# Optimization experiments

Hardware: AMD Instinct MI355X
Metric: run time of the kernel (lower is better)

The kernel has to match this reference:

```python
import jax, jax.numpy as jnp
import numpy as np

LAM = 0.1   # smooth_param
EPS = 1e-8  # torch cosine_similarity eps


def setup_inputs() -> dict:
    key = jax.random.key(0)
    k1, k2, k3 = jax.random.split(key, 3)
    B, num_supp, num_query, T, D = 8, 5, 128, 16, 2048
    supp = jax.random.normal(k1, (B, num_supp, T, D), jnp.float32)
    query = jax.random.normal(k2, (B, num_query, T, D), jnp.float32)
    query_ys = jax.random.randint(k3, (B * num_query,), 0, num_supp)
    return {"supp": supp, "query": query, "query_ys": query_ys}


def _cosine_dist(supp, query):
    # supp: (B, ns, T, D), query: (B, nq, T, D)
    # dist[b,q,s,l,m] = 1 - cos(supp[b,s,l], query[b,q,m]); batch order (b,q,s)
    B, ns, T, D = supp.shape
    nq = query.shape[1]
    dots = jnp.einsum('bsld,bqmd->bqslm', supp, query)
    sn = jnp.linalg.norm(supp, axis=-1)   # (B, ns, T)
    qn = jnp.linalg.norm(query, axis=-1)  # (B, nq, T)
    denom = jnp.maximum(sn[:, None, :, :, None] * qn[:, :, None, None, :], EPS)
    dist = 1.0 - dots / denom
    return dist.reshape(B * nq * ns, T, T)


def _dtw(dist):
    # Relaxed (soft-min) OTAM band DP. dist: (N, T, T) -> (N,)
    # opt grid is (T, T+2) with zero-padded columns m=0 and m=T+1.
    N, T, _ = dist.shape
    dist_pad = jnp.pad(dist, ((0, 0), (0, 0), (1, 1)))  # (N, T, T+2)
    # Row l=0: opt[0,m] = cumsum of dist_pad[0, :m+1]
    row0 = jnp.cumsum(dist_pad[:, 0, :], axis=-1)  # (N, T+2)

    m_idx = jnp.arange(1, T + 2)
    boundary = (m_idx == 1) | (m_idx == T + 1)  # 3-way softmin only at band edges

    def row_step(prev_row, dist_row):
        # prev_row: (N, T+2) = opt[l-1]; dist_row: (N, T+2) = dist_pad[:, l]
        def col_step(left, xs):
            diag, up, d, is_b = xs  # each (N,) except is_b scalar bool
            s2 = jnp.logaddexp(-diag / LAM, -left / LAM)        # {diag, left}
            s3 = jnp.logaddexp(s2, -up / LAM)                   # + {up}
            val = -LAM * jnp.where(is_b, s3, s2) + d
            return val, val

        xs = (prev_row[:, :-1].T, prev_row[:, 1:].T, dist_row[:, 1:].T, boundary)
        init = jnp.zeros((N,), dist_row.dtype)  # opt[l, 0] = 0
        _, cols = jax.lax.scan(col_step, init, xs)  # (T+1, N)
        new_row = jnp.concatenate([init[:, None], cols.T], axis=1)  # (N, T+2)
        return new_row, None

    rows = jnp.swapaxes(dist_pad[:, 1:, :], 0, 1)  # (T-1, N, T+2)
    final_row, _ = jax.lax.scan(row_step, row0, rows)
    return final_row[:, -1]  # opt[:, T-1, T+1]


def _cross_entropy(logits, labels):
    logp = jax.nn.log_softmax(logits, axis=-1)
    return -jnp.mean(jnp.take_along_axis(logp, labels[:, None], axis=1))


def reference(supp, query, query_ys):
    ns = supp.shape[1]
    dist = _cosine_dist(supp, query)            # (B*nq*ns, T, T)
    tam1 = _dtw(dist).reshape(-1, ns)           # forward-direction alignment
    tam2 = _dtw(dist[:, ::-1, ::-1]).reshape(-1, ns)  # flipped (dims 1,2)
    loss1 = _cross_entropy(-tam1, query_ys)
    loss2 = _cross_entropy(-tam2, query_ys)
    loss = 0.5 * (loss1 + loss2)
    tam = 0.5 * (tam1 + tam2)
    return loss, tam
```

## Files before the change

### kernel.cpp

```cpp
#include <hip/hip_runtime.h>
#include <hip/hip_bf16.h>

#define NB   8
#define NS   5
#define NQ   128
#define TT   16
#define DD   2048
#define NROW 1024
#define NSROW (NB * NS * TT)
#define LDB  2056
#define LAMI 10.0f
#define LAMF 0.1f

typedef __attribute__((ext_vector_type(8))) short  short8;
typedef __attribute__((ext_vector_type(4))) float  float4v;

static __device__ __forceinline__ unsigned int f2bf2(float x, float y) {
    union { float f; unsigned int u; } a, b; a.f = x; b.f = y;
    unsigned int ra = a.u + 0x7fffu + ((a.u >> 16) & 1u);
    unsigned int rb = b.u + 0x7fffu + ((b.u >> 16) & 1u);
    return (ra >> 16) | (rb & 0xffff0000u);
}

static __device__ __forceinline__ float lse2f(float x, float y) {
    float mx = fmaxf(x, y), mn = fminf(x, y);
    return mx + __logf(1.0f + __expf(mn - mx));
}

__global__ __launch_bounds__(256) void
preproc_supp(const float* __restrict__ supp, unsigned short* __restrict__ suppBf,
             float* __restrict__ suppSq)
{
    const int wave = threadIdx.x >> 6, lane = threadIdx.x & 63;
    const int row = blockIdx.x * 4 + wave;
    const float* src = supp + (size_t)row * DD;
    unsigned short* dst = suppBf + (size_t)row * DD;
    float ss = 0.f;
    #pragma unroll
    for (int i = 0; i < 8; ++i) {
        float4 v = *reinterpret_cast<const float4*>(src + i * 256 + lane * 4);
        uint2 pv = { f2bf2(v.x, v.y), f2bf2(v.z, v.w) };
        *reinterpret_cast<uint2*>(dst + i * 256 + lane * 4) = pv;
        ss += v.x * v.x + v.y * v.y + v.z * v.z + v.w * v.w;
    }
    #pragma unroll
    for (int off = 32; off >= 1; off >>= 1) ss += __shfl_xor(ss, off, 64);
    if (lane == 0) suppSq[row] = ss;
}

__global__ __launch_bounds__(512, 4) void
dist_dtw_kernel(const unsigned short* __restrict__ suppBf, const float* __restrict__ suppSq,
                const float* __restrict__ query,
                float* __restrict__ out_tam, float* __restrict__ t1w, float* __restrict__ t2w)
{
    __shared__ __align__(16) unsigned short sB[TT * LDB];
    __shared__ float ssq[96];
    __shared__ float distS[NS][TT][TT];
    __shared__ float tamv[16];

    const int tid  = threadIdx.x;
    const int blk  = blockIdx.x;
    const int wave = tid >> 6;
    const int lane = tid & 63;
    const int fr   = lane & 15;
    const int quad = lane >> 4;

    {
        const int r = tid >> 5;
        const int c = tid & 31;
        const float* src = query + (size_t)(blk * TT + r) * DD;
        float ss = 0.f;
        #pragma unroll
        for (int i = 0; i < 16; ++i) {
            float4 v = *reinterpret_cast<const float4*>(src + (c + i * 32) * 4);
            uint2 pv = { f2bf2(v.x, v.y), f2bf2(v.z, v.w) };
            *reinterpret_cast<uint2*>(&sB[r * LDB + (c + i * 32) * 4]) = pv;
            ss += v.x * v.x + v.y * v.y + v.z * v.z + v.w * v.w;
        }
        #pragma unroll
        for (int off = 16; off >= 1; off >>= 1) ss += __shfl_xor(ss, off, 32);
        if ((tid & 31) == 0) ssq[80 + r] = ss;
        if (tid < 80) ssq[tid] = suppSq[(blk >> 7) * (NS * TT) + tid];
    }
    __syncthreads();

    float4v acc0 = {0.f, 0.f, 0.f, 0.f}, acc1 = {0.f, 0.f, 0.f, 0.f};
    if (wave < NS) {
        const unsigned short* ap =
            suppBf + ((size_t)((blk >> 7) * NS + wave) * TT + fr) * DD + quad * 8;
        const unsigned short* bp = &sB[fr * LDB + quad * 8];
        #pragma unroll 8
        for (int k = 0; k < 64; k += 2) {
            short8 a0 = *reinterpret_cast<const short8*>(ap + k * 32);
            short8 a1 = *reinterpret_cast<const short8*>(ap + k * 32 + 32);
            short8 b0 = *reinterpret_cast<const short8*>(bp + k * 32);
            short8 b1 = *reinterpret_cast<const short8*>(bp + k * 32 + 32);
            acc0 = __builtin_amdgcn_mfma_f32_16x16x32_bf16(a0, b0, acc0, 0, 0, 0);
            acc1 = __builtin_amdgcn_mfma_f32_16x16x32_bf16(a1, b1, acc1, 0, 0, 0);
        }
        float qn = sqrtf(ssq[80 + fr]);
        #pragma unroll
        for (int r = 0; r < 4; ++r) {
            int l = quad * 4 + r;
            float denom = fmaxf(sqrtf(ssq[wave * 16 + l]) * qn, 1e-8f);
            distS[wave][l][fr] = 1.0f - (acc0[r] + acc1[r]) / denom;
        }
    }
    __syncthreads();

    if (wave < NS && (lane & 31) <= 17) {
        const int g   = lane & 31;
        const int dir = lane >> 5;
        const int s   = wave;
        float val = 0.f, vprev = 0.f;
        #pragma unroll
        for (int t = 1; t <= 32; ++t) {
            float left = __shfl_up(val,   1, 32);
            float diag = __shfl_up(vprev, 1, 32);
            int l = t - g;
            if (g >= 1 && l >= 0 && l <= 15) {
                float d = 0.f;
                if (g <= 16) d = dir ? distS[s][15 - l][16 - g] : distS[s][l][g - 1];
                float nv;
                if (l == 0) {
                    nv = left + d;
                } else if (g == 1 || g == 17) {
                    nv = -LAMF * lse2f(lse2f(-diag * LAMI, -left * LAMI), -val * LAMI) + d;
                } else {
                    float lo2 = fminf(diag, left), hi2 = fmaxf(diag, left);
                    nv = lo2 - LAMF * __logf(1.0f + __expf((lo2 - hi2) * LAMI)) + d;
                }
                vprev = val; val = nv;
            }
        }
        if (g == 17) tamv[s * 2 + dir] = val;
    }
    __syncthreads();

    if (tid < NS) {
        float t1 = tamv[2 * tid], t2 = tamv[2 * tid + 1];
        int n = blk * NS + tid;
        t1w[n] = t1;
        t2w[n] = t2;
        out_tam[n] = 0.5f * (t1 + t2);
    }
}

__global__ __launch_bounds__(1024) void
loss_kernel(const float* __restrict__ t1w, const float* __restrict__ t2w,
            const int* __restrict__ ys, float* __restrict__ out)
{
    __shared__ float red[16];
    const int row = threadIdx.x;

    float t1[NS], t2[NS];
    #pragma unroll
    for (int s = 0; s < NS; ++s) { t1[s] = t1w[row * NS + s]; t2[s] = t2w[row * NS + s]; }
    const int y = ys[row];

    float mx1 = -t1[0], mx2 = -t2[0];
    #pragma unroll
    for (int s = 1; s < NS; ++s) { mx1 = fmaxf(mx1, -t1[s]); mx2 = fmaxf(mx2, -t2[s]); }
    float s1 = 0.f, s2 = 0.f;
    #pragma unroll
    for (int s = 0; s < NS; ++s) { s1 += __expf(-t1[s] - mx1); s2 += __expf(-t2[s] - mx2); }
    float lse1  = mx1 + __logf(s1);
    float lse2v = mx2 + __logf(s2);

    float ty1 = t1[0], ty2 = t2[0];
    #pragma unroll
    for (int s = 1; s < NS; ++s) { if (y == s) { ty1 = t1[s]; ty2 = t2[s]; } }

    float c = 0.5f * ((lse1 + ty1) + (lse2v + ty2));

    #pragma unroll
    for (int off = 32; off >= 1; off >>= 1) c += __shfl_down(c, off, 64);
    if ((row & 63) == 0) red[row >> 6] = c;
    __syncthreads();
    if (row == 0) {
        float tot = 0.f;
        #pragma unroll
        for (int i = 0; i < 16; ++i) tot += red[i];
        out[0] = tot * (1.0f / (float)NROW);
    }
}

extern "C" void kernel_launch(void* const* d_in, const int* in_sizes, int n_in,
                              void* d_out, int out_size, void* d_ws, size_t ws_size,
                              hipStream_t stream) {
    const float* supp  = (const float*)d_in[0];
    const float* query = (const float*)d_in[1];
    const int*   ys    = (const int*)d_in[2];
    float* out = (float*)d_out;

    float* t1w    = (float*)d_ws;
    float* t2w    = t1w + NROW * NS;
    float* suppSq = t2w + NROW * NS;
    unsigned short* suppBf = (unsigned short*)(suppSq + NSROW);

    preproc_supp<<<NSROW / 4, 256, 0, stream>>>(supp, suppBf, suppSq);
    dist_dtw_kernel<<<NROW, 512, 0, stream>>>(suppBf, suppSq, query, out + 1, t1w, t2w);
    loss_kernel<<<1, 1024, 0, stream>>>(t1w, t2w, ys, out);
}
```

Measured before the change: 254.6 us.

## Halve query LDS staging to raise occupancy and fuse loss via atomics

The query tile is now staged in LDS in two halves of the D dimension rather than all at once. This halves the shared-memory footprint so the launch bound can allow 8 blocks per CU instead of 4, at the cost of extra barriers between the two halves. The separate loss kernel is removed. Each DTW block computes its row's cross-entropy term and atomically adds it to the output, which preproc_supp zeroes first. This saves a launch and a workspace round trip, but the floating-point atomics make the summation order nondeterministic.

```diff
diff --git a/kernel.cpp b/kernel.cpp
--- a/kernel.cpp
+++ b/kernel.cpp
@@ -8,7 +8,7 @@
 #define DD   2048
 #define NROW 1024
 #define NSROW (NB * NS * TT)
-#define LDB  2056
+#define LDB  1032
 #define LAMI 10.0f
 #define LAMF 0.1f
 
@@ -29,8 +29,9 @@
 
 __global__ __launch_bounds__(256) void
 preproc_supp(const float* __restrict__ supp, unsigned short* __restrict__ suppBf,
-             float* __restrict__ suppSq)
+             float* __restrict__ suppSq, float* __restrict__ loss0)
 {
+    if (blockIdx.x == 0 && threadIdx.x == 0) loss0[0] = 0.f;
     const int wave = threadIdx.x >> 6, lane = threadIdx.x & 63;
     const int row = blockIdx.x * 4 + wave;
     const float* src = supp + (size_t)row * DD;
@@ -48,10 +49,10 @@
     if (lane == 0) suppSq[row] = ss;
 }
 
-__global__ __launch_bounds__(512, 4) void
+__global__ __launch_bounds__(512, 8) void
 dist_dtw_kernel(const unsigned short* __restrict__ suppBf, const float* __restrict__ suppSq,
-                const float* __restrict__ query,
-                float* __restrict__ out_tam, float* __restrict__ t1w, float* __restrict__ t2w)
+                const float* __restrict__ query, const int* __restrict__ ys,
+                float* __restrict__ out)
 {
     __shared__ __align__(16) unsigned short sB[TT * LDB];
     __shared__ float ssq[96];
@@ -65,36 +66,65 @@
     const int fr   = lane & 15;
     const int quad = lane >> 4;
 
+    const int qr = tid >> 5;
+    const int qc = tid & 31;
+    const float* qsrc = query + (size_t)(blk * TT + qr) * DD;
+
     {
-        const int r = tid >> 5;
-        const int c = tid & 31;
-        const float* src = query + (size_t)(blk * TT + r) * DD;
         float ss = 0.f;
         #pragma unroll
-        for (int i = 0; i < 16; ++i) {
-            float4 v = *reinterpret_cast<const float4*>(src + (c + i * 32) * 4);
+        for (int i = 0; i < 8; ++i) {
+            float4 v = *reinterpret_cast<const float4*>(qsrc + (qc + i * 32) * 4);
             uint2 pv = { f2bf2(v.x, v.y), f2bf2(v.z, v.w) };
-            *reinterpret_cast<uint2*>(&sB[r * LDB + (c + i * 32) * 4]) = pv;
+            *reinterpret_cast<uint2*>(&sB[qr * LDB + (qc + i * 32) * 4]) = pv;
             ss += v.x * v.x + v.y * v.y + v.z * v.z + v.w * v.w;
         }
         #pragma unroll
         for (int off = 16; off >= 1; off >>= 1) ss += __shfl_xor(ss, off, 32);
-        if ((tid & 31) == 0) ssq[80 + r] = ss;
+        if (qc == 0) ssq[80 + qr] = ss;
         if (tid < 80) ssq[tid] = suppSq[(blk >> 7) * (NS * TT) + tid];
     }
     __syncthreads();
 
     float4v acc0 = {0.f, 0.f, 0.f, 0.f}, acc1 = {0.f, 0.f, 0.f, 0.f};
+    const unsigned short* ap =
+        suppBf + ((size_t)((blk >> 7) * NS + wave) * TT + fr) * DD + quad * 8;
+    const unsigned short* bp = &sB[fr * LDB + quad * 8];
     if (wave < NS) {
-        const unsigned short* ap =
-            suppBf + ((size_t)((blk >> 7) * NS + wave) * TT + fr) * DD + quad * 8;
-        const unsigned short* bp = &sB[fr * LDB + quad * 8];
         #pragma unroll 8
-        for (int k = 0; k < 64; k += 2) {
+        for (int k = 0; k < 32; k += 2) {
             short8 a0 = *reinterpret_cast<const short8*>(ap + k * 32);
             short8 a1 = *reinterpret_cast<const short8*>(ap + k * 32 + 32);
             short8 b0 = *reinterpret_cast<const short8*>(bp + k * 32);
             short8 b1 = *reinterpret_cast<const short8*>(bp + k * 32 + 32);
+            acc0 = __builtin_amdgcn_mfma_f32_16x16x32_bf16(a0, b0, acc0, 0, 0, 0);
+            acc1 = __builtin_amdgcn_mfma_f32_16x16x32_bf16(a1, b1, acc1, 0, 0, 0);
+        }
+    }
+    __syncthreads();
+
+    {
+        float ss = 0.f;
+        #pragma unroll
+        for (int i = 0; i < 8; ++i) {
+            float4 v = *reinterpret_cast<const float4*>(qsrc + 1024 + (qc + i * 32) * 4);
+            uint2 pv = { f2bf2(v.x, v.y), f2bf2(v.z, v.w) };
+            *reinterpret_cast<uint2*>(&sB[qr * LDB + (qc + i * 32) * 4]) = pv;
+            ss += v.x * v.x + v.y * v.y + v.z * v.z + v.w * v.w;
+        }
+        #pragma unroll
+        for (int off = 16; off >= 1; off >>= 1) ss += __shfl_xor(ss, off, 32);
+        if (qc == 0) ssq[80 + qr] += ss;
+    }
+    __syncthreads();
+
+    if (wave < NS) {
+        #pragma unroll 8
+        for (int k = 32; k < 64; k += 2) {
+            short8 a0 = *reinterpret_cast<const short8*>(ap + k * 32);
+            short8 a1 = *reinterpret_cast<const short8*>(ap + k * 32 + 32);
+            short8 b0 = *reinterpret_cast<const short8*>(bp + (k - 32) * 32);
+            short8 b1 = *reinterpret_cast<const short8*>(bp + (k - 32) * 32 + 32);
             acc0 = __builtin_amdgcn_mfma_f32_16x16x32_bf16(a0, b0, acc0, 0, 0, 0);
             acc1 = __builtin_amdgcn_mfma_f32_16x16x32_bf16(a1, b1, acc1, 0, 0, 0);
         }
@@ -138,50 +168,29 @@
     __syncthreads();
 
     if (tid < NS) {
-        float t1 = tamv[2 * tid], t2 = tamv[2 * tid + 1];
-        int n = blk * NS + tid;
-        t1w[n] = t1;
-        t2w[n] = t2;
-        out_tam[n] = 0.5f * (t1 + t2);
-    }
-}
-
-__global__ __launch_bounds__(1024) void
-loss_kernel(const float* __restrict__ t1w, const float* __restrict__ t2w,
-            const int* __restrict__ ys, float* __restrict__ out)
-{
-    __shared__ float red[16];
-    const int row = threadIdx.x;
-
-    float t1[NS], t2[NS];
-    #pragma unroll
-    for (int s = 0; s < NS; ++s) { t1[s] = t1w[row * NS + s]; t2[s] = t2w[row * NS + s]; }
-    const int y = ys[row];
-
-    float mx1 = -t1[0], mx2 = -t2[0];
-    #pragma unroll
-    for (int s = 1; s < NS; ++s) { mx1 = fmaxf(mx1, -t1[s]); mx2 = fmaxf(mx2, -t2[s]); }
-    float s1 = 0.f, s2 = 0.f;
-    #pragma unroll
-    for (int s = 0; s < NS; ++s) { s1 += __expf(-t1[s] - mx1); s2 += __expf(-t2[s] - mx2); }
-    float lse1  = mx1 + __logf(s1);
-    float lse2v = mx2 + __logf(s2);
-
-    float ty1 = t1[0], ty2 = t2[0];
-    #pragma unroll
-    for (int s = 1; s < NS; ++s) { if (y == s) { ty1 = t1[s]; ty2 = t2[s]; } }
-
-    float c = 0.5f * ((lse1 + ty1) + (lse2v + ty2));
-
-    #pragma unroll
-    for (int off = 32; off >= 1; off >>= 1) c += __shfl_down(c, off, 64);
-    if ((row & 63) == 0) red[row >> 6] = c;
-    __syncthreads();
-    if (row == 0) {
-        float tot = 0.f;
-        #pragma unroll
-        for (int i = 0; i < 16; ++i) tot += red[i];
-        out[0] = tot * (1.0f / (float)NROW);
+        out[1 + blk * NS + tid] = 0.5f * (tamv[2 * tid] + tamv[2 * tid + 1]);
+    }
+    if (tid == 0) {
+        float t1v[NS], t2v[NS];
+        #pragma unroll
+        for (int s = 0; s < NS; ++s) { t1v[s] = tamv[2 * s]; t2v[s] = tamv[2 * s + 1]; }
+        const int y = ys[blk];
+
+        float mx1 = -t1v[0], mx2 = -t2v[0];
+        #pragma unroll
+        for (int s = 1; s < NS; ++s) { mx1 = fmaxf(mx1, -t1v[s]); mx2 = fmaxf(mx2, -t2v[s]); }
+        float s1 = 0.f, s2 = 0.f;
+        #pragma unroll
+        for (int s = 0; s < NS; ++s) { s1 += __expf(-t1v[s] - mx1); s2 += __expf(-t2v[s] - mx2); }
+        float lse1  = mx1 + __logf(s1);
+        float lse2v = mx2 + __logf(s2);
+
+        float ty1 = t1v[0], ty2 = t2v[0];
+        #pragma unroll
+        for (int s = 1; s < NS; ++s) { if (y == s) { ty1 = t1v[s]; ty2 = t2v[s]; } }
+
+        float c = 0.5f * ((lse1 + ty1) + (lse2v + ty2));
+        atomicAdd(out, c * (1.0f / (float)NROW));
     }
 }
 
@@ -193,12 +202,9 @@
     const int*   ys    = (const int*)d_in[2];
     float* out = (float*)d_out;
 
-    float* t1w    = (float*)d_ws;
-    float* t2w    = t1w + NROW * NS;
-    float* suppSq = t2w + NROW * NS;
+    float* suppSq = (float*)d_ws;
     unsigned short* suppBf = (unsigned short*)(suppSq + NSROW);
 
-    preproc_supp<<<NSROW / 4, 256, 0, stream>>>(supp, suppBf, suppSq);
-    dist_dtw_kernel<<<NROW, 512, 0, stream>>>(suppBf, suppSq, query, out + 1, t1w, t2w);
-    loss_kernel<<<1, 1024, 0, stream>>>(t1w, t2w, ys, out);
-}
+    preproc_supp<<<NSROW / 4, 256, 0, stream>>>(supp, suppBf, suppSq, out);
+    dist_dtw_kernel<<<NROW, 512, 0, stream>>>(suppBf, suppSq, query, ys, out);
+}
```

New measurement: 230.2 us. 1.11x faster.
